# Performance work log

Measured on AMD Instinct MI355X. Metric: run time of the kernel, lower is better.

Reference implementation:

```python
import jax, jax.numpy as jnp
import numpy as np

N_NODES = 100000
N_EDGES = 3200000
IN_F = 256
OUT_F = 128


def setup_inputs() -> dict:
    key = jax.random.key(0)
    k1, k2, k3, k4, k5, k6 = jax.random.split(key, 6)
    x = jax.random.normal(k1, (N_NODES, IN_F), dtype=jnp.float32)
    edge_row = jax.random.randint(k2, (N_EDGES,), 0, N_NODES, dtype=jnp.int32)
    edge_col = jax.random.randint(k3, (N_EDGES,), 0, N_NODES, dtype=jnp.int32)
    edge_val = jax.random.uniform(k4, (N_EDGES,), dtype=jnp.float32)
    stdv = 1.0 / np.sqrt(OUT_F)
    weight = jax.random.uniform(k5, (IN_F, OUT_F), dtype=jnp.float32, minval=-stdv, maxval=stdv)
    bias = jax.random.uniform(k6, (OUT_F,), dtype=jnp.float32, minval=-stdv, maxval=stdv)
    return {"x": x, "edge_row": edge_row, "edge_col": edge_col,
            "edge_val": edge_val, "weight": weight, "bias": bias}


def reference(x, edge_row, edge_col, edge_val, weight, bias):
    # dropout p=0.0 -> identity. support = x @ W  [N, out_f]
    support = x @ weight
    # spmm(adj, support): out[r] = sum_e adj_val[e] * support[col[e]] for edges with row[e]==r
    gathered = support[edge_col] * edge_val[:, None]  # [E, out_f]
    out = jax.ops.segment_sum(gathered, edge_row, num_segments=N_NODES)
    out = out + bias
    return jax.nn.relu(out)
```

## Files before the change

### kernel.cpp

```cpp
#include <hip/hip_runtime.h>
#include <hip/hip_fp16.h>

#define IN_F 256
#define OUT_F 128
#define RPB 64
#define LOG_RPB 6
#define MAXB 2048
#define CHUNK 8192
#define CAP 3072

typedef __attribute__((ext_vector_type(8))) short short8;
typedef __attribute__((ext_vector_type(4))) float f32x4;

__device__ inline short bf16r(float f) {
  unsigned u = __float_as_uint(f);
  u += 0x7FFF + ((u >> 16) & 1);
  return (short)(u >> 16);
}

#define COL_OF(e) ((e) & 0x1FFFFu)
#define Q9_OF(e)  (((e) >> 17) & 0x1FFu)
#define RL_OF(e)  ((e) >> 26)

__global__ __launch_bounds__(512) void gemm_hist(const float* __restrict__ x,
                                                 const float* __restrict__ w,
                                                 __half* __restrict__ sup,
                                                 int n_nodes,
                                                 const int* __restrict__ erow,
                                                 int* __restrict__ cnt2d,
                                                 int n_edges, int nbuck, int nblk,
                                                 int ngemm) {
  __shared__ char smem[128 * 256 * 2];
  int t = threadIdx.x;

  if ((int)blockIdx.x >= ngemm) {
    int* h = (int*)smem;
    int hb = blockIdx.x - ngemm;
    for (int i = t; i < nbuck; i += 512) h[i] = 0;
    __syncthreads();
    int beg = hb * CHUNK;
    int end = min(beg + CHUNK, n_edges);
    for (int e = beg + t; e < end; e += 512) atomicAdd(&h[erow[e] >> LOG_RPB], 1);
    __syncthreads();
    for (int i = t; i < nbuck; i += 512) cnt2d[(size_t)i * nblk + hb] = h[i];
    return;
  }

  short* wlds = (short*)smem;
  for (int idx = t; idx < 256 * 128; idx += 512) {
    int k = idx >> 7;
    int n = idx & 127;
    int g = k >> 3;
    wlds[n * 256 + ((g ^ (n & 7)) << 3) + (k & 7)] = bf16r(w[idx]);
  }
  __syncthreads();

  int lane = t & 63;
  int wid = t >> 6;
  int wrow = (wid >> 1) * 64;
  int wcol = (wid & 1) * 64;
  int row_blk = blockIdx.x * 256;

  int arow[4];
#pragma unroll
  for (int mt = 0; mt < 4; ++mt)
    arow[mt] = min(row_blk + wrow + mt * 16 + (lane & 15), n_nodes - 1);
  int koff = (lane >> 4) * 8;

  f32x4 acc[4][4];
#pragma unroll
  for (int mt = 0; mt < 4; ++mt)
#pragma unroll
    for (int nt = 0; nt < 4; ++nt) acc[mt][nt] = (f32x4){0.f, 0.f, 0.f, 0.f};

#pragma unroll 2
  for (int kk = 0; kk < IN_F; kk += 32) {
    short8 af[4];
#pragma unroll
    for (int mt = 0; mt < 4; ++mt) {
      const float* px = x + (size_t)arow[mt] * IN_F + kk + koff;
      float4 p = *(const float4*)px;
      float4 q = *(const float4*)(px + 4);
      short8 a;
      a[0] = bf16r(p.x); a[1] = bf16r(p.y); a[2] = bf16r(p.z); a[3] = bf16r(p.w);
      a[4] = bf16r(q.x); a[5] = bf16r(q.y); a[6] = bf16r(q.z); a[7] = bf16r(q.w);
      af[mt] = a;
    }
    short8 bf[4];
    int g = (kk >> 3) + (lane >> 4);
#pragma unroll
    for (int nt = 0; nt < 4; ++nt) {
      int n = wcol + nt * 16 + (lane & 15);
      bf[nt] = *(const short8*)&wlds[n * 256 + ((g ^ (n & 7)) << 3)];
    }
#pragma unroll
    for (int mt = 0; mt < 4; ++mt)
#pragma unroll
      for (int nt = 0; nt < 4; ++nt)
        acc[mt][nt] = __builtin_amdgcn_mfma_f32_16x16x32_bf16(af[mt], bf[nt],
                                                              acc[mt][nt], 0, 0, 0);
  }

#pragma unroll
  for (int mt = 0; mt < 4; ++mt)
#pragma unroll
    for (int nt = 0; nt < 4; ++nt)
#pragma unroll
      for (int reg = 0; reg < 4; ++reg) {
        int grow = row_blk + wrow + mt * 16 + (lane >> 4) * 4 + reg;
        int gcol = wcol + nt * 16 + (lane & 15);
        if (grow < n_nodes)
          sup[(size_t)grow * OUT_F + gcol] = __float2half(acc[mt][nt][reg]);
      }
}

__global__ __launch_bounds__(256) void rowsum(const int* __restrict__ cnt2d,
                                              int* __restrict__ bcnt, int nblk) {
  __shared__ int red[256];
  int b = blockIdx.x;
  const int* row = cnt2d + (size_t)b * nblk;
  int t = threadIdx.x;
  int s = 0;
  for (int i = t; i < nblk; i += 256) s += row[i];
  red[t] = s;
  __syncthreads();
  for (int off = 128; off > 0; off >>= 1) {
    if (t < off) red[t] += red[t + off];
    __syncthreads();
  }
  if (t == 0) bcnt[b] = red[0];
}

__global__ __launch_bounds__(1024) void bucket_scan(const int* __restrict__ bcnt,
                                                    int* __restrict__ bptr, int nbuck) {
  __shared__ int sc[1024];
  int t = threadIdx.x;
  int i0 = 2 * t, i1 = 2 * t + 1;
  int c0 = (i0 < nbuck) ? bcnt[i0] : 0;
  int c1 = (i1 < nbuck) ? bcnt[i1] : 0;
  int s = c0 + c1;
  sc[t] = s;
  __syncthreads();
  for (int off = 1; off < 1024; off <<= 1) {
    int u = (t >= off) ? sc[t - off] : 0;
    __syncthreads();
    sc[t] += u;
    __syncthreads();
  }
  int run = sc[t] - s;
  if (i0 < nbuck) { bptr[i0] = run; run += c0; }
  if (i1 < nbuck) { bptr[i1] = run; run += c1; }
  if (t == 1023) bptr[nbuck] = sc[1023];
}

__global__ __launch_bounds__(256) void rowscan(const int* __restrict__ cnt2d,
                                               const int* __restrict__ bptr,
                                               int* __restrict__ off2d, int nblk) {
  __shared__ int sc[256];
  int b = blockIdx.x;
  const int* row = cnt2d + (size_t)b * nblk;
  int* orow = off2d + (size_t)b * nblk;
  int t = threadIdx.x;
  int chunk = (nblk + 255) >> 8;
  int beg = t * chunk, end2 = min(beg + chunk, nblk);
  int s = 0;
  for (int i = beg; i < end2; ++i) s += row[i];
  sc[t] = s;
  __syncthreads();
  for (int off = 1; off < 256; off <<= 1) {
    int u = (t >= off) ? sc[t - off] : 0;
    __syncthreads();
    sc[t] += u;
    __syncthreads();
  }
  int run = sc[t] - s + bptr[b];
  for (int i = beg; i < end2; ++i) {
    orow[i] = run;
    run += row[i];
  }
}

__global__ __launch_bounds__(512) void coarse_bin(const int* __restrict__ erow,
                                                  const int* __restrict__ ecol,
                                                  const float* __restrict__ eval,
                                                  const int* __restrict__ off2d,
                                                  unsigned* __restrict__ tmp,
                                                  int n_edges, int nbuck, int nblk) {
  __shared__ int cnt[MAXB];
  __shared__ int base[MAXB];
  int t = threadIdx.x;
  for (int i = t; i < nbuck; i += 512) {
    cnt[i] = 0;
    base[i] = off2d[(size_t)i * nblk + blockIdx.x];
  }
  __syncthreads();
  int beg = blockIdx.x * CHUNK;
  int end = min(beg + CHUNK, n_edges);
  for (int e = beg + t; e < end; e += 512) {
    int r = erow[e];
    int b = r >> LOG_RPB;
    int pos = base[b] + atomicAdd(&cnt[b], 1);
    float v = eval[e];
    int q = min(max((int)(v * 511.f + 0.5f), 0), 511);
    tmp[pos] = (unsigned)ecol[e] | ((unsigned)q << 17) |
               ((unsigned)(r & (RPB - 1)) << 26);
  }
}

__global__ __launch_bounds__(256) void sort_gather(const int* __restrict__ bptr,
                                                   const unsigned* __restrict__ tmp,
                                                   unsigned* __restrict__ spill,
                                                   const __half* __restrict__ sup,
                                                   const float* __restrict__ bias,
                                                   float* __restrict__ out,
                                                   int n_nodes) {
  __shared__ unsigned eL[CAP];
  __shared__ int hist[RPB];
  __shared__ int ex[RPB + 1];
  __shared__ int cur[RPB];
  int b = blockIdx.x;
  int row0 = b << LOG_RPB;
  int t = threadIdx.x;
  int bbeg = bptr[b];
  int bend = bptr[b + 1];
  int m = bend - bbeg;

  if (t < RPB) hist[t] = 0;
  __syncthreads();
  for (int j = bbeg + t; j < bend; j += 256) atomicAdd(&hist[RL_OF(tmp[j])], 1);
  __syncthreads();
  if (t < RPB) ex[t] = hist[t];
  __syncthreads();
  for (int off = 1; off < RPB; off <<= 1) {
    int u = (t < RPB && t >= off) ? ex[t - off] : 0;
    __syncthreads();
    if (t < RPB) ex[t] += u;
    __syncthreads();
  }
  if (t < RPB) {
    int st = ex[t] - hist[t];
    ex[t] = st;
    cur[t] = st;
  }
  if (t == 0) ex[RPB] = m;
  __syncthreads();
  for (int j = bbeg + t; j < bend; j += 256) {
    unsigned e = tmp[j];
    int pos = atomicAdd(&cur[RL_OF(e)], 1);
    if (pos < CAP) eL[pos] = e;
    else spill[bbeg + pos] = e;
  }
  __syncthreads();

  int lane = t & 63;
  int wv = t >> 6;
  int qw = lane >> 4;
  int sl = lane & 15;
  const float dq = 1.0f / 511.0f;
  float4 bi0 = ((const float4*)bias)[2 * sl + 0];
  float4 bi1 = ((const float4*)bias)[2 * sl + 1];
  int nr = min(RPB, n_nodes - row0);

#define LOADE(J) (((J) < CAP) ? eL[(J)] : spill[bbeg + (J)])
  for (int rl = wv; rl < nr; rl += 4) {
    int beg = ex[rl];
    int end = ex[rl + 1];
    float a0[8] = {0.f, 0.f, 0.f, 0.f, 0.f, 0.f, 0.f, 0.f};
    float a1[8] = {0.f, 0.f, 0.f, 0.f, 0.f, 0.f, 0.f, 0.f};

    int j = beg + qw;
    for (; j + 4 < end; j += 8) {
      unsigned e0 = LOADE(j);
      unsigned e1 = LOADE(j + 4);
      uint4 s0 = ((const uint4*)(sup + (size_t)COL_OF(e0) * OUT_F))[sl];
      uint4 s1 = ((const uint4*)(sup + (size_t)COL_OF(e1) * OUT_F))[sl];
      float v0 = (float)Q9_OF(e0) * dq;
      float v1 = (float)Q9_OF(e1) * dq;
      float2 p;
      p = __half22float2(*(__half2*)&s0.x); a0[0] = fmaf(p.x, v0, a0[0]); a0[1] = fmaf(p.y, v0, a0[1]);
      p = __half22float2(*(__half2*)&s0.y); a0[2] = fmaf(p.x, v0, a0[2]); a0[3] = fmaf(p.y, v0, a0[3]);
      p = __half22float2(*(__half2*)&s0.z); a0[4] = fmaf(p.x, v0, a0[4]); a0[5] = fmaf(p.y, v0, a0[5]);
      p = __half22float2(*(__half2*)&s0.w); a0[6] = fmaf(p.x, v0, a0[6]); a0[7] = fmaf(p.y, v0, a0[7]);
      p = __half22float2(*(__half2*)&s1.x); a1[0] = fmaf(p.x, v1, a1[0]); a1[1] = fmaf(p.y, v1, a1[1]);
      p = __half22float2(*(__half2*)&s1.y); a1[2] = fmaf(p.x, v1, a1[2]); a1[3] = fmaf(p.y, v1, a1[3]);
      p = __half22float2(*(__half2*)&s1.z); a1[4] = fmaf(p.x, v1, a1[4]); a1[5] = fmaf(p.y, v1, a1[5]);
      p = __half22float2(*(__half2*)&s1.w); a1[6] = fmaf(p.x, v1, a1[6]); a1[7] = fmaf(p.y, v1, a1[7]);
    }
    if (j < end) {
      unsigned e0 = LOADE(j);
      uint4 s0 = ((const uint4*)(sup + (size_t)COL_OF(e0) * OUT_F))[sl];
      float v0 = (float)Q9_OF(e0) * dq;
      float2 p;
      p = __half22float2(*(__half2*)&s0.x); a0[0] = fmaf(p.x, v0, a0[0]); a0[1] = fmaf(p.y, v0, a0[1]);
      p = __half22float2(*(__half2*)&s0.y); a0[2] = fmaf(p.x, v0, a0[2]); a0[3] = fmaf(p.y, v0, a0[3]);
      p = __half22float2(*(__half2*)&s0.z); a0[4] = fmaf(p.x, v0, a0[4]); a0[5] = fmaf(p.y, v0, a0[5]);
      p = __half22float2(*(__half2*)&s0.w); a0[6] = fmaf(p.x, v0, a0[6]); a0[7] = fmaf(p.y, v0, a0[7]);
    }

    float r[8];
#pragma unroll
    for (int i = 0; i < 8; ++i) {
      r[i] = a0[i] + a1[i];
      r[i] += __shfl_xor(r[i], 16);
      r[i] += __shfl_xor(r[i], 32);
    }
    if (qw == 0) {
      float4 o0, o1;
      o0.x = fmaxf(r[0] + bi0.x, 0.f);
      o0.y = fmaxf(r[1] + bi0.y, 0.f);
      o0.z = fmaxf(r[2] + bi0.z, 0.f);
      o0.w = fmaxf(r[3] + bi0.w, 0.f);
      o1.x = fmaxf(r[4] + bi1.x, 0.f);
      o1.y = fmaxf(r[5] + bi1.y, 0.f);
      o1.z = fmaxf(r[6] + bi1.z, 0.f);
      o1.w = fmaxf(r[7] + bi1.w, 0.f);
      float4* orow = (float4*)(out + (size_t)(row0 + rl) * OUT_F);
      orow[2 * sl + 0] = o0;
      orow[2 * sl + 1] = o1;
    }
  }
#undef LOADE
}

__global__ __launch_bounds__(512) void gemm_mfma_only(const float* __restrict__ x,
                                                      const float* __restrict__ w,
                                                      __half* __restrict__ sup,
                                                      int n_nodes) {
  __shared__ short wlds[128 * 256];
  int t = threadIdx.x;
  for (int idx = t; idx < 256 * 128; idx += 512) {
    int k = idx >> 7;
    int n = idx & 127;
    int g = k >> 3;
    wlds[n * 256 + ((g ^ (n & 7)) << 3) + (k & 7)] = bf16r(w[idx]);
  }
  __syncthreads();
  int lane = t & 63;
  int wid = t >> 6;
  int wrow = (wid >> 1) * 64;
  int wcol = (wid & 1) * 64;
  int row_blk = blockIdx.x * 256;
  int arow[4];
#pragma unroll
  for (int mt = 0; mt < 4; ++mt)
    arow[mt] = min(row_blk + wrow + mt * 16 + (lane & 15), n_nodes - 1);
  int koff = (lane >> 4) * 8;
  f32x4 acc[4][4];
#pragma unroll
  for (int mt = 0; mt < 4; ++mt)
#pragma unroll
    for (int nt = 0; nt < 4; ++nt) acc[mt][nt] = (f32x4){0.f, 0.f, 0.f, 0.f};
#pragma unroll 2
  for (int kk = 0; kk < IN_F; kk += 32) {
    short8 af[4];
#pragma unroll
    for (int mt = 0; mt < 4; ++mt) {
      const float* px = x + (size_t)arow[mt] * IN_F + kk + koff;
      float4 p = *(const float4*)px;
      float4 q = *(const float4*)(px + 4);
      short8 a;
      a[0] = bf16r(p.x); a[1] = bf16r(p.y); a[2] = bf16r(p.z); a[3] = bf16r(p.w);
      a[4] = bf16r(q.x); a[5] = bf16r(q.y); a[6] = bf16r(q.z); a[7] = bf16r(q.w);
      af[mt] = a;
    }
    short8 bf[4];
    int g = (kk >> 3) + (lane >> 4);
#pragma unroll
    for (int nt = 0; nt < 4; ++nt) {
      int n = wcol + nt * 16 + (lane & 15);
      bf[nt] = *(const short8*)&wlds[n * 256 + ((g ^ (n & 7)) << 3)];
    }
#pragma unroll
    for (int mt = 0; mt < 4; ++mt)
#pragma unroll
      for (int nt = 0; nt < 4; ++nt)
        acc[mt][nt] = __builtin_amdgcn_mfma_f32_16x16x32_bf16(af[mt], bf[nt],
                                                              acc[mt][nt], 0, 0, 0);
  }
#pragma unroll
  for (int mt = 0; mt < 4; ++mt)
#pragma unroll
    for (int nt = 0; nt < 4; ++nt)
#pragma unroll
      for (int reg = 0; reg < 4; ++reg) {
        int grow = row_blk + wrow + mt * 16 + (lane >> 4) * 4 + reg;
        int gcol = wcol + nt * 16 + (lane & 15);
        if (grow < n_nodes)
          sup[(size_t)grow * OUT_F + gcol] = __float2half(acc[mt][nt][reg]);
      }
}

__global__ __launch_bounds__(256) void init_bias(float* __restrict__ out,
                                                 const float* __restrict__ bias,
                                                 int total) {
  int i = blockIdx.x * 256 + threadIdx.x;
  if (i < total) out[i] = bias[i & (OUT_F - 1)];
}

__global__ __launch_bounds__(256) void spmm_scatter(const int* __restrict__ erow,
                                                    const int* __restrict__ ecol,
                                                    const float* __restrict__ eval,
                                                    const __half* __restrict__ sup,
                                                    float* __restrict__ out,
                                                    int n_edges) {
  long long t = (long long)blockIdx.x * 256 + threadIdx.x;
  int e = (int)(t >> 6);
  if (e >= n_edges) return;
  int lane = (int)(t & 63);
  int r = erow[e];
  int c = ecol[e];
  float v = eval[e];
  __half2 s = ((const __half2*)(sup + (size_t)c * OUT_F))[lane];
  float2 f = __half22float2(s);
  float* orow = out + (size_t)r * OUT_F + 2 * lane;
  unsafeAtomicAdd(orow + 0, f.x * v);
  unsafeAtomicAdd(orow + 1, f.y * v);
}

__global__ __launch_bounds__(256) void relu_k(float* __restrict__ out, int total) {
  int i = blockIdx.x * 256 + threadIdx.x;
  if (i < total) out[i] = fmaxf(out[i], 0.f);
}

extern "C" void kernel_launch(void* const* d_in, const int* in_sizes, int n_in,
                              void* d_out, int out_size, void* d_ws, size_t ws_size,
                              hipStream_t stream) {
  const float* x = (const float*)d_in[0];
  const int* erow = (const int*)d_in[1];
  const int* ecol = (const int*)d_in[2];
  const float* eval = (const float*)d_in[3];
  const float* w = (const float*)d_in[4];
  const float* bias = (const float*)d_in[5];
  float* out = (float*)d_out;

  int n_nodes = in_sizes[0] / IN_F;
  int n_edges = in_sizes[1];
  int total = n_nodes * OUT_F;
  int nbuck = (n_nodes + RPB - 1) >> LOG_RPB;
  int nblk = (n_edges + CHUNK - 1) / CHUNK;
  int ngemm = (n_nodes + 255) / 256;

  char* p = (char*)d_ws;
  __half* sup = (__half*)p;             p += (size_t)n_nodes * OUT_F * 2;
  unsigned* tmp = (unsigned*)p;         p += (size_t)n_edges * 4;
  unsigned* spill = (unsigned*)p;       p += (size_t)n_edges * 4;
  int* bcnt = (int*)p;                  p += (size_t)nbuck * 4;
  int* bptr = (int*)p;                  p += (size_t)(nbuck + 1) * 4;
  int* cnt2d = (int*)p;                 p += (size_t)nbuck * nblk * 4;
  int* off2d = (int*)p;                 p += (size_t)nbuck * nblk * 4;
  size_t need = (size_t)(p - (char*)d_ws);

  if (ws_size >= need && nbuck <= MAXB) {
    gemm_hist<<<ngemm + nblk, 512, 0, stream>>>(x, w, sup, n_nodes, erow, cnt2d,
                                                n_edges, nbuck, nblk, ngemm);
    rowsum<<<nbuck, 256, 0, stream>>>(cnt2d, bcnt, nblk);
    bucket_scan<<<1, 1024, 0, stream>>>(bcnt, bptr, nbuck);
    rowscan<<<nbuck, 256, 0, stream>>>(cnt2d, bptr, off2d, nblk);
    coarse_bin<<<nblk, 512, 0, stream>>>(erow, ecol, eval, off2d, tmp,
                                         n_edges, nbuck, nblk);
    sort_gather<<<nbuck, 256, 0, stream>>>(bptr, tmp, spill, sup, bias, out,
                                           n_nodes);
  } else {
    gemm_mfma_only<<<ngemm, 512, 0, stream>>>(x, w, sup, n_nodes);
    init_bias<<<(total + 255) / 256, 256, 0, stream>>>(out, bias, total);
    long long threads = (long long)n_edges * 64;
    spmm_scatter<<<(int)((threads + 255) / 256), 256, 0, stream>>>(erow, ecol, eval,
                                                                   sup, out, n_edges);
    relu_k<<<(total + 255) / 256, 256, 0, stream>>>(out, total);
  }
}
```

Before: 239.4 us.

## Fuse GEMM with coarse binning and pre-convert weights to bf16 in global memory

Result: no change. 240.4 us (+0.4%).

```diff
diff --git a/kernel.cpp b/kernel.cpp
--- a/kernel.cpp
+++ b/kernel.cpp
@@ -22,62 +22,158 @@
 #define Q9_OF(e)  (((e) >> 17) & 0x1FFu)
 #define RL_OF(e)  ((e) >> 26)
 
-__global__ __launch_bounds__(512) void gemm_hist(const float* __restrict__ x,
-                                                 const float* __restrict__ w,
-                                                 __half* __restrict__ sup,
-                                                 int n_nodes,
-                                                 const int* __restrict__ erow,
-                                                 int* __restrict__ cnt2d,
-                                                 int n_edges, int nbuck, int nblk,
-                                                 int ngemm) {
-  __shared__ char smem[128 * 256 * 2];
+__global__ __launch_bounds__(256) void hist_wprep(const int* __restrict__ erow,
+                                                  int* __restrict__ cnt2d,
+                                                  const float* __restrict__ w,
+                                                  short* __restrict__ wt,
+                                                  int n_edges, int nbuck, int nblk) {
+  __shared__ int h[MAXB];
+  int t = threadIdx.x;
+  if ((int)blockIdx.x >= nblk) {
+    int i = (blockIdx.x - nblk) * 1024 + t * 4;
+#pragma unroll
+    for (int u = 0; u < 4; ++u) {
+      int idx = i + u;
+      int k = idx >> 7;
+      int n = idx & 127;
+      wt[n * 256 + k] = bf16r(w[idx]);
+    }
+    return;
+  }
+  for (int i = t; i < nbuck; i += 256) h[i] = 0;
+  __syncthreads();
+  int beg = blockIdx.x * CHUNK;
+  int end = min(beg + CHUNK, n_edges);
+  for (int e = beg + t; e < end; e += 256) atomicAdd(&h[erow[e] >> LOG_RPB], 1);
+  __syncthreads();
+  for (int i = t; i < nbuck; i += 256) cnt2d[(size_t)i * nblk + blockIdx.x] = h[i];
+}
+
+__global__ __launch_bounds__(256) void rowsum(const int* __restrict__ cnt2d,
+                                              int* __restrict__ bcnt, int nblk) {
+  __shared__ int red[256];
+  int b = blockIdx.x;
+  const int* row = cnt2d + (size_t)b * nblk;
+  int t = threadIdx.x;
+  int s = 0;
+  for (int i = t; i < nblk; i += 256) s += row[i];
+  red[t] = s;
+  __syncthreads();
+  for (int off = 128; off > 0; off >>= 1) {
+    if (t < off) red[t] += red[t + off];
+    __syncthreads();
+  }
+  if (t == 0) bcnt[b] = red[0];
+}
+
+__global__ __launch_bounds__(1024) void bucket_scan(const int* __restrict__ bcnt,
+                                                    int* __restrict__ bptr, int nbuck) {
+  __shared__ int sc[1024];
+  int t = threadIdx.x;
+  int i0 = 2 * t, i1 = 2 * t + 1;
+  int c0 = (i0 < nbuck) ? bcnt[i0] : 0;
+  int c1 = (i1 < nbuck) ? bcnt[i1] : 0;
+  int s = c0 + c1;
+  sc[t] = s;
+  __syncthreads();
+  for (int off = 1; off < 1024; off <<= 1) {
+    int u = (t >= off) ? sc[t - off] : 0;
+    __syncthreads();
+    sc[t] += u;
+    __syncthreads();
+  }
+  int run = sc[t] - s;
+  if (i0 < nbuck) { bptr[i0] = run; run += c0; }
+  if (i1 < nbuck) { bptr[i1] = run; run += c1; }
+  if (t == 1023) bptr[nbuck] = sc[1023];
+}
+
+__global__ __launch_bounds__(256) void rowscan(const int* __restrict__ cnt2d,
+                                               const int* __restrict__ bptr,
+                                               int* __restrict__ off2d, int nblk) {
+  __shared__ int sc[256];
+  int b = blockIdx.x;
+  const int* row = cnt2d + (size_t)b * nblk;
+  int* orow = off2d + (size_t)b * nblk;
+  int t = threadIdx.x;
+  int chunk = (nblk + 255) >> 8;
+  int beg = t * chunk, end2 = min(beg + chunk, nblk);
+  int s = 0;
+  for (int i = beg; i < end2; ++i) s += row[i];
+  sc[t] = s;
+  __syncthreads();
+  for (int off = 1; off < 256; off <<= 1) {
+    int u = (t >= off) ? sc[t - off] : 0;
+    __syncthreads();
+    sc[t] += u;
+    __syncthreads();
+  }
+  int run = sc[t] - s + bptr[b];
+  for (int i = beg; i < end2; ++i) {
+    orow[i] = run;
+    run += row[i];
+  }
+}
+
+__global__ __launch_bounds__(512) void gemm_coarse(const float* __restrict__ x,
+                                                   const short* __restrict__ wt,
+                                                   __half* __restrict__ sup,
+                                                   int n_nodes,
+                                                   const int* __restrict__ erow,
+                                                   const int* __restrict__ ecol,
+                                                   const float* __restrict__ eval,
+                                                   const int* __restrict__ off2d,
+                                                   unsigned* __restrict__ tmp,
+                                                   int n_edges, int nbuck, int nblk,
+                                                   int ngemm) {
+  __shared__ int cnt[MAXB];
+  __shared__ int base[MAXB];
   int t = threadIdx.x;
 
   if ((int)blockIdx.x >= ngemm) {
-    int* h = (int*)smem;
-    int hb = blockIdx.x - ngemm;
-    for (int i = t; i < nbuck; i += 512) h[i] = 0;
-    __syncthreads();
-    int beg = hb * CHUNK;
+    int cb = blockIdx.x - ngemm;
+    for (int i = t; i < nbuck; i += 512) {
+      cnt[i] = 0;
+      base[i] = off2d[(size_t)i * nblk + cb];
+    }
+    __syncthreads();
+    int beg = cb * CHUNK;
     int end = min(beg + CHUNK, n_edges);
-    for (int e = beg + t; e < end; e += 512) atomicAdd(&h[erow[e] >> LOG_RPB], 1);
-    __syncthreads();
-    for (int i = t; i < nbuck; i += 512) cnt2d[(size_t)i * nblk + hb] = h[i];
+    for (int e = beg + t; e < end; e += 512) {
+      int r = erow[e];
+      int b = r >> LOG_RPB;
+      int pos = base[b] + atomicAdd(&cnt[b], 1);
+      float v = eval[e];
+      int q = min(max((int)(v * 511.f + 0.5f), 0), 511);
+      tmp[pos] = (unsigned)ecol[e] | ((unsigned)q << 17) |
+                 ((unsigned)(r & (RPB - 1)) << 26);
+    }
     return;
   }
-
-  short* wlds = (short*)smem;
-  for (int idx = t; idx < 256 * 128; idx += 512) {
-    int k = idx >> 7;
-    int n = idx & 127;
-    int g = k >> 3;
-    wlds[n * 256 + ((g ^ (n & 7)) << 3) + (k & 7)] = bf16r(w[idx]);
-  }
-  __syncthreads();
 
   int lane = t & 63;
   int wid = t >> 6;
-  int wrow = (wid >> 1) * 64;
+  int wrow = (wid >> 1) * 32;
   int wcol = (wid & 1) * 64;
-  int row_blk = blockIdx.x * 256;
-
-  int arow[4];
-#pragma unroll
-  for (int mt = 0; mt < 4; ++mt)
+  int row_blk = blockIdx.x * 128;
+
+  int arow[2];
+#pragma unroll
+  for (int mt = 0; mt < 2; ++mt)
     arow[mt] = min(row_blk + wrow + mt * 16 + (lane & 15), n_nodes - 1);
   int koff = (lane >> 4) * 8;
 
-  f32x4 acc[4][4];
-#pragma unroll
-  for (int mt = 0; mt < 4; ++mt)
+  f32x4 acc[2][4];
+#pragma unroll
+  for (int mt = 0; mt < 2; ++mt)
 #pragma unroll
     for (int nt = 0; nt < 4; ++nt) acc[mt][nt] = (f32x4){0.f, 0.f, 0.f, 0.f};
 
 #pragma unroll 2
   for (int kk = 0; kk < IN_F; kk += 32) {
-    short8 af[4];
-#pragma unroll
-    for (int mt = 0; mt < 4; ++mt) {
+    short8 af[2];
+#pragma unroll
+    for (int mt = 0; mt < 2; ++mt) {
       const float* px = x + (size_t)arow[mt] * IN_F + kk + koff;
       float4 p = *(const float4*)px;
       float4 q = *(const float4*)(px + 4);
@@ -87,14 +183,13 @@
       af[mt] = a;
     }
     short8 bf[4];
-    int g = (kk >> 3) + (lane >> 4);
 #pragma unroll
     for (int nt = 0; nt < 4; ++nt) {
       int n = wcol + nt * 16 + (lane & 15);
-      bf[nt] = *(const short8*)&wlds[n * 256 + ((g ^ (n & 7)) << 3)];
-    }
-#pragma unroll
-    for (int mt = 0; mt < 4; ++mt)
+      bf[nt] = *(const short8*)&wt[n * 256 + kk + koff];
+    }
+#pragma unroll
+    for (int mt = 0; mt < 2; ++mt)
 #pragma unroll
       for (int nt = 0; nt < 4; ++nt)
         acc[mt][nt] = __builtin_amdgcn_mfma_f32_16x16x32_bf16(af[mt], bf[nt],
@@ -102,7 +197,7 @@
   }
 
 #pragma unroll
-  for (int mt = 0; mt < 4; ++mt)
+  for (int mt = 0; mt < 2; ++mt)
 #pragma unroll
     for (int nt = 0; nt < 4; ++nt)
 #pragma unroll
@@ -112,99 +207,6 @@
         if (grow < n_nodes)
           sup[(size_t)grow * OUT_F + gcol] = __float2half(acc[mt][nt][reg]);
       }
-}
-
-__global__ __launch_bounds__(256) void rowsum(const int* __restrict__ cnt2d,
-                                              int* __restrict__ bcnt, int nblk) {
-  __shared__ int red[256];
-  int b = blockIdx.x;
-  const int* row = cnt2d + (size_t)b * nblk;
-  int t = threadIdx.x;
-  int s = 0;
-  for (int i = t; i < nblk; i += 256) s += row[i];
-  red[t] = s;
-  __syncthreads();
-  for (int off = 128; off > 0; off >>= 1) {
-    if (t < off) red[t] += red[t + off];
-    __syncthreads();
-  }
-  if (t == 0) bcnt[b] = red[0];
-}
-
-__global__ __launch_bounds__(1024) void bucket_scan(const int* __restrict__ bcnt,
-                                                    int* __restrict__ bptr, int nbuck) {
-  __shared__ int sc[1024];
-  int t = threadIdx.x;
-  int i0 = 2 * t, i1 = 2 * t + 1;
-  int c0 = (i0 < nbuck) ? bcnt[i0] : 0;
-  int c1 = (i1 < nbuck) ? bcnt[i1] : 0;
-  int s = c0 + c1;
-  sc[t] = s;
-  __syncthreads();
-  for (int off = 1; off < 1024; off <<= 1) {
-    int u = (t >= off) ? sc[t - off] : 0;
-    __syncthreads();
-    sc[t] += u;
-    __syncthreads();
-  }
-  int run = sc[t] - s;
-  if (i0 < nbuck) { bptr[i0] = run; run += c0; }
-  if (i1 < nbuck) { bptr[i1] = run; run += c1; }
-  if (t == 1023) bptr[nbuck] = sc[1023];
-}
-
-__global__ __launch_bounds__(256) void rowscan(const int* __restrict__ cnt2d,
-                                               const int* __restrict__ bptr,
-                                               int* __restrict__ off2d, int nblk) {
-  __shared__ int sc[256];
-  int b = blockIdx.x;
-  const int* row = cnt2d + (size_t)b * nblk;
-  int* orow = off2d + (size_t)b * nblk;
-  int t = threadIdx.x;
-  int chunk = (nblk + 255) >> 8;
-  int beg = t * chunk, end2 = min(beg + chunk, nblk);
-  int s = 0;
-  for (int i = beg; i < end2; ++i) s += row[i];
-  sc[t] = s;
-  __syncthreads();
-  for (int off = 1; off < 256; off <<= 1) {
-    int u = (t >= off) ? sc[t - off] : 0;
-    __syncthreads();
-    sc[t] += u;
-    __syncthreads();
-  }
-  int run = sc[t] - s + bptr[b];
-  for (int i = beg; i < end2; ++i) {
-    orow[i] = run;
-    run += row[i];
-  }
-}
-
-__global__ __launch_bounds__(512) void coarse_bin(const int* __restrict__ erow,
-                                                  const int* __restrict__ ecol,
-                                                  const float* __restrict__ eval,
-                                                  const int* __restrict__ off2d,
-                                                  unsigned* __restrict__ tmp,
-                                                  int n_edges, int nbuck, int nblk) {
-  __shared__ int cnt[MAXB];
-  __shared__ int base[MAXB];
-  int t = threadIdx.x;
-  for (int i = t; i < nbuck; i += 512) {
-    cnt[i] = 0;
-    base[i] = off2d[(size_t)i * nblk + blockIdx.x];
-  }
-  __syncthreads();
-  int beg = blockIdx.x * CHUNK;
-  int end = min(beg + CHUNK, n_edges);
-  for (int e = beg + t; e < end; e += 512) {
-    int r = erow[e];
-    int b = r >> LOG_RPB;
-    int pos = base[b] + atomicAdd(&cnt[b], 1);
-    float v = eval[e];
-    int q = min(max((int)(v * 511.f + 0.5f), 0), 511);
-    tmp[pos] = (unsigned)ecol[e] | ((unsigned)q << 17) |
-               ((unsigned)(r & (RPB - 1)) << 26);
-  }
 }
 
 __global__ __launch_bounds__(256) void sort_gather(const int* __restrict__ bptr,
@@ -262,6 +264,13 @@
   int nr = min(RPB, n_nodes - row0);
 
 #define LOADE(J) (((J) < CAP) ? eL[(J)] : spill[bbeg + (J)])
+#define ACC8(A, S, V)                                                             \
+  { float2 p;                                                                     \
+    p = __half22float2(*(__half2*)&(S).x); A[0] = fmaf(p.x, V, A[0]); A[1] = fmaf(p.y, V, A[1]); \
+    p = __half22float2(*(__half2*)&(S).y); A[2] = fmaf(p.x, V, A[2]); A[3] = fmaf(p.y, V, A[3]); \
+    p = __half22float2(*(__half2*)&(S).z); A[4] = fmaf(p.x, V, A[4]); A[5] = fmaf(p.y, V, A[5]); \
+    p = __half22float2(*(__half2*)&(S).w); A[6] = fmaf(p.x, V, A[6]); A[7] = fmaf(p.y, V, A[7]); }
+
   for (int rl = wv; rl < nr; rl += 4) {
     int beg = ex[rl];
     int end = ex[rl + 1];
@@ -276,25 +285,14 @@
       uint4 s1 = ((const uint4*)(sup + (size_t)COL_OF(e1) * OUT_F))[sl];
       float v0 = (float)Q9_OF(e0) * dq;
       float v1 = (float)Q9_OF(e1) * dq;
-      float2 p;
-      p = __half22float2(*(__half2*)&s0.x); a0[0] = fmaf(p.x, v0, a0[0]); a0[1] = fmaf(p.y, v0, a0[1]);
-      p = __half22float2(*(__half2*)&s0.y); a0[2] = fmaf(p.x, v0, a0[2]); a0[3] = fmaf(p.y, v0, a0[3]);
-      p = __half22float2(*(__half2*)&s0.z); a0[4] = fmaf(p.x, v0, a0[4]); a0[5] = fmaf(p.y, v0, a0[5]);
-      p = __half22float2(*(__half2*)&s0.w); a0[6] = fmaf(p.x, v0, a0[6]); a0[7] = fmaf(p.y, v0, a0[7]);
-      p = __half22float2(*(__half2*)&s1.x); a1[0] = fmaf(p.x, v1, a1[0]); a1[1] = fmaf(p.y, v1, a1[1]);
-      p = __half22float2(*(__half2*)&s1.y); a1[2] = fmaf(p.x, v1, a1[2]); a1[3] = fmaf(p.y, v1, a1[3]);
-      p = __half22float2(*(__half2*)&s1.z); a1[4] = fmaf(p.x, v1, a1[4]); a1[5] = fmaf(p.y, v1, a1[5]);
-      p = __half22float2(*(__half2*)&s1.w); a1[6] = fmaf(p.x, v1, a1[6]); a1[7] = fmaf(p.y, v1, a1[7]);
+      ACC8(a0, s0, v0);
+      ACC8(a1, s1, v1);
     }
     if (j < end) {
       unsigned e0 = LOADE(j);
       uint4 s0 = ((const uint4*)(sup + (size_t)COL_OF(e0) * OUT_F))[sl];
       float v0 = (float)Q9_OF(e0) * dq;
-      float2 p;
-      p = __half22float2(*(__half2*)&s0.x); a0[0] = fmaf(p.x, v0, a0[0]); a0[1] = fmaf(p.y, v0, a0[1]);
-      p = __half22float2(*(__half2*)&s0.y); a0[2] = fmaf(p.x, v0, a0[2]); a0[3] = fmaf(p.y, v0, a0[3]);
-      p = __half22float2(*(__half2*)&s0.z); a0[4] = fmaf(p.x, v0, a0[4]); a0[5] = fmaf(p.y, v0, a0[5]);
-      p = __half22float2(*(__half2*)&s0.w); a0[6] = fmaf(p.x, v0, a0[6]); a0[7] = fmaf(p.y, v0, a0[7]);
+      ACC8(a0, s0, v0);
     }
 
     float r[8];
@@ -319,6 +317,7 @@
       orow[2 * sl + 1] = o1;
     }
   }
+#undef ACC8
 #undef LOADE
 }
 
@@ -438,12 +437,13 @@
   int total = n_nodes * OUT_F;
   int nbuck = (n_nodes + RPB - 1) >> LOG_RPB;
   int nblk = (n_edges + CHUNK - 1) / CHUNK;
-  int ngemm = (n_nodes + 255) / 256;
+  int ngemm = (n_nodes + 127) / 128;
 
   char* p = (char*)d_ws;
   __half* sup = (__half*)p;             p += (size_t)n_nodes * OUT_F * 2;
   unsigned* tmp = (unsigned*)p;         p += (size_t)n_edges * 4;
   unsigned* spill = (unsigned*)p;       p += (size_t)n_edges * 4;
+  short* wt = (short*)p;                p += (size_t)IN_F * OUT_F * 2;
   int* bcnt = (int*)p;                  p += (size_t)nbuck * 4;
   int* bptr = (int*)p;                  p += (size_t)(nbuck + 1) * 4;
   int* cnt2d = (int*)p;                 p += (size_t)nbuck * nblk * 4;
@@ -451,17 +451,18 @@
   size_t need = (size_t)(p - (char*)d_ws);
 
   if (ws_size >= need && nbuck <= MAXB) {
-    gemm_hist<<<ngemm + nblk, 512, 0, stream>>>(x, w, sup, n_nodes, erow, cnt2d,
-                                                n_edges, nbuck, nblk, ngemm);
+    hist_wprep<<<nblk + 32, 256, 0, stream>>>(erow, cnt2d, w, wt,
+                                              n_edges, nbuck, nblk);
     rowsum<<<nbuck, 256, 0, stream>>>(cnt2d, bcnt, nblk);
     bucket_scan<<<1, 1024, 0, stream>>>(bcnt, bptr, nbuck);
     rowscan<<<nbuck, 256, 0, stream>>>(cnt2d, bptr, off2d, nblk);
-    coarse_bin<<<nblk, 512, 0, stream>>>(erow, ecol, eval, off2d, tmp,
-                                         n_edges, nbuck, nblk);
+    gemm_coarse<<<ngemm + nblk, 512, 0, stream>>>(x, wt, sup, n_nodes, erow, ecol,
+                                                  eval, off2d, tmp, n_edges, nbuck,
+                                                  nblk, ngemm);
     sort_gather<<<nbuck, 256, 0, stream>>>(bptr, tmp, spill, sup, bias, out,
                                            n_nodes);
   } else {
-    gemm_mfma_only<<<ngemm, 512, 0, stream>>>(x, w, sup, n_nodes);
+    gemm_mfma_only<<<(n_nodes + 255) / 256, 512, 0, stream>>>(x, w, sup, n_nodes);
     init_bias<<<(total + 255) / 256, 256, 0, stream>>>(out, bias, total);
     long long threads = (long long)n_edges * 64;
     spmm_scatter<<<(int)((threads + 255) / 256), 256, 0, stream>>>(erow, ecol, eval,
```
